# Optimization experiments

Measured on AMD Instinct MI355X. Metric: run time of the kernel, lower is better.

Reference implementation:

```python
import jax, jax.numpy as jnp
import numpy as np

TEMP = 0.2
EPS = 1e-12  # F.normalize eps


def setup_inputs() -> dict:
    key = jax.random.key(0)
    k1, k2 = jax.random.split(key)
    l, B, K, D = 4, 64, 32, 128
    emb_i = jax.random.normal(k1, (l, B, K, D), dtype=jnp.float32)
    emb_j = jax.random.normal(k2, (l, B, K, D), dtype=jnp.float32)
    joint_valid = jnp.ones((B, K), dtype=jnp.float32)
    return {"emb_i": emb_i, "emb_j": emb_j, "joint_valid": joint_valid}


def _l2norm(x):
    n = jnp.sqrt(jnp.sum(x * x, axis=-1, keepdims=True))
    return x / jnp.maximum(n, EPS)


def reference(emb_i, emb_j, joint_valid):
    l, B, K, D = emb_i.shape
    N = B * K
    z_i = _l2norm(emb_i.reshape(l, N, D))
    z_j = _l2norm(emb_j.reshape(l, N, D))
    reps = jnp.concatenate([z_i, z_j], axis=1)              # (l, 2N, D), unit rows
    # cosine similarity of unit vectors == matmul
    sim = jnp.einsum('lnd,lmd->lnm', reps, reps)            # (l, 2N, 2N)
    idx = jnp.arange(N)
    pos = sim[:, idx, idx + N]                              # diag offset +N, (l, N)
    # note: original code uses the SAME +N offset diagonal for both ij and ji
    positives = jnp.concatenate([pos, pos], axis=1)         # (l, 2N)
    neg_mask = 1.0 - jnp.eye(2 * N, dtype=sim.dtype)        # (2N, 2N)
    denom = jnp.sum(neg_mask[None] * jnp.exp(sim / TEMP), axis=2)  # (l, 2N)
    loss_partial = -jnp.log(jnp.exp(positives / TEMP) / denom)    # (l, 2N)
    joints_mask = joint_valid.reshape(1, 1, B, K)
    all_num = jnp.sum(joint_valid)
    loss = jnp.sum(loss_partial.reshape(l, 2, B, K) * joints_mask) / (2.0 * all_num)
    return loss
```

## Files before the change

kernel.cpp:

```cpp
#include <hip/hip_runtime.h>
#include <hip/hip_bf16.h>

typedef __attribute__((ext_vector_type(8))) short short8;
typedef __attribute__((ext_vector_type(4))) float floatx4;

#define NROWS 4096
#define NHALF 2048
#define DDIM  128
#define LDST  136
#define SQRT_SCALE 2.6857914f
#define LN2 0.69314718056f

#define WS_ROWSUM_OFF 64
#define WS_DIAG_OFF   16448
#define WS_POS_OFF    32832
#define WS_Z_BYTE_OFF 196864

__device__ inline unsigned short f2bf(float f) {
    unsigned u = __builtin_bit_cast(unsigned, f);
    u += 0x7fffu + ((u >> 16) & 1u);
    return (unsigned short)(u >> 16);
}

__global__ __launch_bounds__(256) void k_norm(const float* __restrict__ emb_i,
                                              const float* __restrict__ emb_j,
                                              const float* __restrict__ jv,
                                              float* __restrict__ wsf,
                                              unsigned short* __restrict__ z) {
    int bx = blockIdx.x, tid = threadIdx.x;
    if (bx == 4096) {
        __shared__ float sred[256];
        float s = 0.f;
        #pragma unroll
        for (int i = 0; i < 8; ++i) s += jv[tid + 256 * i];
        sred[tid] = s; __syncthreads();
        for (int off = 128; off > 0; off >>= 1) {
            if (tid < off) sred[tid] += sred[tid + off];
            __syncthreads();
        }
        if (tid == 0) wsf[1] = sred[0];
        return;
    }
    int gid = bx * 256 + tid;
    if (gid == 0) wsf[0] = 0.f;
    if (gid >= WS_ROWSUM_OFF && gid < WS_ROWSUM_OFF + 16384) wsf[gid] = 0.f;

    int wave = tid >> 6, lane = tid & 63;
    int r = bx * 4 + wave;
    int l = r >> 12, n = r & 4095;
    const float* src = (n < NHALF) ? (emb_i + ((size_t)l * NHALF + n) * DDIM)
                                   : (emb_j + ((size_t)l * NHALF + (n - NHALF)) * DDIM);
    float2 v = *(const float2*)(src + lane * 2);
    float ss = v.x * v.x + v.y * v.y;
    #pragma unroll
    for (int off = 1; off < 64; off <<= 1) ss += __shfl_xor(ss, off);
    float inv = SQRT_SCALE / fmaxf(sqrtf(ss), 1e-12f);
    unsigned pack = ((unsigned)f2bf(v.y * inv) << 16) | (unsigned)f2bf(v.x * inv);
    *(unsigned*)(z + (size_t)r * DDIM + lane * 2) = pack;
}

__global__ __launch_bounds__(256) void k_sim(const unsigned short* __restrict__ z,
                                             float* __restrict__ rowsum,
                                             float* __restrict__ diag,
                                             float* __restrict__ pos) {
    __shared__ __align__(16) unsigned short lds[128 * LDST];
    int bx = blockIdx.x, tid = threadIdx.x;
    int l = bx & 3, rb = (bx >> 2) & 15, cb = bx >> 6;
    int wave = tid >> 6, lane = tid & 63, m = lane & 15, quad = lane >> 4;
    const unsigned short* zl = z + (size_t)l * NROWS * DDIM;
    int l4 = l * NROWS;
    int wr0 = rb * 256 + wave * 64;

    short8 a[4][4];
    #pragma unroll
    for (int rs = 0; rs < 4; ++rs) {
        const unsigned short* p = zl + (size_t)(wr0 + rs * 16 + m) * DDIM + quad * 8;
        #pragma unroll
        for (int kk = 0; kk < 4; ++kk) a[rs][kk] = *(const short8*)(p + kk * 32);
    }
    floatx4 rsum[4];
    #pragma unroll
    for (int rs = 0; rs < 4; ++rs) rsum[rs] = (floatx4){0.f, 0.f, 0.f, 0.f};

    for (int stg = 0; stg < 4; ++stg) {
        int cg0 = cb * 512 + stg * 128;
        __syncthreads();
        #pragma unroll
        for (int i = 0; i < 8; ++i) {
            int chunk = tid + 256 * i;
            int col = chunk >> 4, off = chunk & 15;
            uint4 d = *(const uint4*)(zl + (size_t)(cg0 + col) * DDIM + off * 8);
            *(uint4*)&lds[col * LDST + off * 8] = d;
        }
        __syncthreads();
        #pragma unroll
        for (int cs = 0; cs < 8; ++cs) {
            int ct = cg0 + cs * 16;
            const unsigned short* lp = &lds[(cs * 16 + m) * LDST + quad * 8];
            short8 b0 = *(const short8*)(lp);
            short8 b1 = *(const short8*)(lp + 32);
            short8 b2 = *(const short8*)(lp + 64);
            short8 b3 = *(const short8*)(lp + 96);
            #pragma unroll
            for (int rs = 0; rs < 4; ++rs) {
                floatx4 acc = (floatx4){0.f, 0.f, 0.f, 0.f};
                acc = __builtin_amdgcn_mfma_f32_16x16x32_bf16(a[rs][0], b0, acc, 0, 0, 0);
                acc = __builtin_amdgcn_mfma_f32_16x16x32_bf16(a[rs][1], b1, acc, 0, 0, 0);
                acc = __builtin_amdgcn_mfma_f32_16x16x32_bf16(a[rs][2], b2, acc, 0, 0, 0);
                acc = __builtin_amdgcn_mfma_f32_16x16x32_bf16(a[rs][3], b3, acc, 0, 0, 0);
                int rowbase = wr0 + rs * 16;
                bool isdiag = (ct == rowbase);
                bool ispos  = (ct == (rowbase ^ 2048));
                if (isdiag || ispos) {
                    int c = m - (quad << 2);
                    if (c >= 0 && c < 4) {
                        float v = acc[c];
                        float* dst = isdiag ? &diag[l4 + rowbase + m]
                                            : &pos[l4 + rowbase + m];
                        *dst = v;
                    }
                }
                #pragma unroll
                for (int c = 0; c < 4; ++c)
                    rsum[rs][c] += __builtin_amdgcn_exp2f(acc[c]);
            }
        }
    }
    #pragma unroll
    for (int off = 1; off < 16; off <<= 1)
        #pragma unroll
        for (int rs = 0; rs < 4; ++rs)
            #pragma unroll
            for (int c = 0; c < 4; ++c)
                rsum[rs][c] += __shfl_xor(rsum[rs][c], off);
    if (m == 0) {
        #pragma unroll
        for (int rs = 0; rs < 4; ++rs)
            #pragma unroll
            for (int c = 0; c < 4; ++c) {
                int rg = wr0 + rs * 16 + quad * 4 + c;
                atomicAdd(&rowsum[l4 + rg], rsum[rs][c]);
            }
    }
}

__global__ __launch_bounds__(256) void k_loss(const float* __restrict__ jv,
                                              const float* __restrict__ rowsum,
                                              const float* __restrict__ diag,
                                              const float* __restrict__ pos,
                                              float* __restrict__ wsf) {
    __shared__ float sred[256];
    int tid = threadIdx.x;
    int r = blockIdx.x * 256 + tid;
    int n = r & 4095;
    float denom = rowsum[r] - __builtin_amdgcn_exp2f(diag[r]);
    float contrib = LN2 * (__builtin_amdgcn_logf(denom) - pos[r]);
    float local = contrib * jv[n & (NHALF - 1)];
    sred[tid] = local; __syncthreads();
    for (int off = 128; off > 0; off >>= 1) {
        if (tid < off) sred[tid] += sred[tid + off];
        __syncthreads();
    }
    if (tid == 0) atomicAdd(&wsf[0], sred[0]);
}

__global__ void k_final(const float* __restrict__ wsf, float* __restrict__ out) {
    if (threadIdx.x == 0) out[0] = wsf[0] / (2.f * wsf[1]);
}

extern "C" void kernel_launch(void* const* d_in, const int* in_sizes, int n_in,
                              void* d_out, int out_size, void* d_ws, size_t ws_size,
                              hipStream_t stream) {
    const float* emb_i = (const float*)d_in[0];
    const float* emb_j = (const float*)d_in[1];
    const float* jv    = (const float*)d_in[2];
    float* wsf    = (float*)d_ws;
    float* rowsum = wsf + WS_ROWSUM_OFF;
    float* diag   = wsf + WS_DIAG_OFF;
    float* pos    = wsf + WS_POS_OFF;
    unsigned short* z = (unsigned short*)((char*)d_ws + WS_Z_BYTE_OFF);
    float* out = (float*)d_out;

    k_norm <<<4097, 256, 0, stream>>>(emb_i, emb_j, jv, wsf, z);
    k_sim  <<<512,  256, 0, stream>>>(z, rowsum, diag, pos);
    k_loss <<<64,   256, 0, stream>>>(jv, rowsum, diag, pos, wsf);
    k_final<<<1,    64,  0, stream>>>(wsf, out);
}
```

Baseline: 99.83 us.

## Exploit similarity symmetry by computing only upper-triangular tiles with column sums

The similarity kernel now enumerates only the upper-triangular 256x256 tiles per layer. Each off-diagonal tile adds its exp values both into row sums and, through LDS atomics, into column sums, so each mirrored tile is computed once. This roughly halves the MFMA and exp work, at the cost of extra shuffles and shared and global atomics. The normalize kernel also processes two rows per wave with float4 loads to cut its block count.

```diff
diff --git a/kernel.cpp b/kernel.cpp
--- a/kernel.cpp
+++ b/kernel.cpp
@@ -28,7 +28,7 @@
                                               float* __restrict__ wsf,
                                               unsigned short* __restrict__ z) {
     int bx = blockIdx.x, tid = threadIdx.x;
-    if (bx == 4096) {
+    if (bx == 2048) {
         __shared__ float sred[256];
         float s = 0.f;
         #pragma unroll
@@ -45,18 +45,19 @@
     if (gid == 0) wsf[0] = 0.f;
     if (gid >= WS_ROWSUM_OFF && gid < WS_ROWSUM_OFF + 16384) wsf[gid] = 0.f;
 
-    int wave = tid >> 6, lane = tid & 63;
-    int r = bx * 4 + wave;
+    int wave = tid >> 6, lane = tid & 63, half = lane >> 5, sl = lane & 31;
+    int r = bx * 8 + wave * 2 + half;
     int l = r >> 12, n = r & 4095;
     const float* src = (n < NHALF) ? (emb_i + ((size_t)l * NHALF + n) * DDIM)
                                    : (emb_j + ((size_t)l * NHALF + (n - NHALF)) * DDIM);
-    float2 v = *(const float2*)(src + lane * 2);
-    float ss = v.x * v.x + v.y * v.y;
-    #pragma unroll
-    for (int off = 1; off < 64; off <<= 1) ss += __shfl_xor(ss, off);
+    float4 v = *(const float4*)(src + sl * 4);
+    float ss = v.x * v.x + v.y * v.y + v.z * v.z + v.w * v.w;
+    #pragma unroll
+    for (int off = 1; off < 32; off <<= 1) ss += __shfl_xor(ss, off);
     float inv = SQRT_SCALE / fmaxf(sqrtf(ss), 1e-12f);
-    unsigned pack = ((unsigned)f2bf(v.y * inv) << 16) | (unsigned)f2bf(v.x * inv);
-    *(unsigned*)(z + (size_t)r * DDIM + lane * 2) = pack;
+    unsigned p0 = ((unsigned)f2bf(v.y * inv) << 16) | (unsigned)f2bf(v.x * inv);
+    unsigned p1 = ((unsigned)f2bf(v.w * inv) << 16) | (unsigned)f2bf(v.z * inv);
+    *(uint2*)(z + (size_t)r * DDIM + sl * 4) = (uint2){p0, p1};
 }
 
 __global__ __launch_bounds__(256) void k_sim(const unsigned short* __restrict__ z,
@@ -64,12 +65,21 @@
                                              float* __restrict__ diag,
                                              float* __restrict__ pos) {
     __shared__ __align__(16) unsigned short lds[128 * LDST];
+    __shared__ float colsum[256];
     int bx = blockIdx.x, tid = threadIdx.x;
-    int l = bx & 3, rb = (bx >> 2) & 15, cb = bx >> 6;
+    int l = bx & 3, t = bx >> 2;
+    int rb = 0;
+    while (t >= 16 - rb) { t -= 16 - rb; ++rb; }
+    int cb = rb + t;
+    bool offdiag = (cb != rb);
+    bool isposT  = (cb == (rb ^ 8));
+    int R = rb * 256, C = cb * 256;
     int wave = tid >> 6, lane = tid & 63, m = lane & 15, quad = lane >> 4;
     const unsigned short* zl = z + (size_t)l * NROWS * DDIM;
     int l4 = l * NROWS;
-    int wr0 = rb * 256 + wave * 64;
+    int wr0 = R + wave * 64;
+
+    colsum[tid] = 0.f;
 
     short8 a[4][4];
     #pragma unroll
@@ -82,8 +92,8 @@
     #pragma unroll
     for (int rs = 0; rs < 4; ++rs) rsum[rs] = (floatx4){0.f, 0.f, 0.f, 0.f};
 
-    for (int stg = 0; stg < 4; ++stg) {
-        int cg0 = cb * 512 + stg * 128;
+    for (int stg = 0; stg < 2; ++stg) {
+        int cg0 = C + stg * 128;
         __syncthreads();
         #pragma unroll
         for (int i = 0; i < 8; ++i) {
@@ -95,12 +105,13 @@
         __syncthreads();
         #pragma unroll
         for (int cs = 0; cs < 8; ++cs) {
-            int ct = cg0 + cs * 16;
+            int lc = stg * 128 + cs * 16;
             const unsigned short* lp = &lds[(cs * 16 + m) * LDST + quad * 8];
             short8 b0 = *(const short8*)(lp);
             short8 b1 = *(const short8*)(lp + 32);
             short8 b2 = *(const short8*)(lp + 64);
             short8 b3 = *(const short8*)(lp + 96);
+            float cacc = 0.f;
             #pragma unroll
             for (int rs = 0; rs < 4; ++rs) {
                 floatx4 acc = (floatx4){0.f, 0.f, 0.f, 0.f};
@@ -108,21 +119,30 @@
                 acc = __builtin_amdgcn_mfma_f32_16x16x32_bf16(a[rs][1], b1, acc, 0, 0, 0);
                 acc = __builtin_amdgcn_mfma_f32_16x16x32_bf16(a[rs][2], b2, acc, 0, 0, 0);
                 acc = __builtin_amdgcn_mfma_f32_16x16x32_bf16(a[rs][3], b3, acc, 0, 0, 0);
-                int rowbase = wr0 + rs * 16;
-                bool isdiag = (ct == rowbase);
-                bool ispos  = (ct == (rowbase ^ 2048));
-                if (isdiag || ispos) {
+                int lr = wave * 64 + rs * 16;
+                if (lr == lc) {
                     int c = m - (quad << 2);
                     if (c >= 0 && c < 4) {
                         float v = acc[c];
-                        float* dst = isdiag ? &diag[l4 + rowbase + m]
-                                            : &pos[l4 + rowbase + m];
-                        *dst = v;
+                        if (!offdiag) diag[l4 + R + lr + m] = v;
+                        else if (isposT) {
+                            pos[l4 + R + lr + m] = v;
+                            pos[l4 + C + lr + m] = v;
+                        }
                     }
                 }
-                #pragma unroll
-                for (int c = 0; c < 4; ++c)
-                    rsum[rs][c] += __builtin_amdgcn_exp2f(acc[c]);
+                float e0 = __builtin_amdgcn_exp2f(acc[0]);
+                float e1 = __builtin_amdgcn_exp2f(acc[1]);
+                float e2 = __builtin_amdgcn_exp2f(acc[2]);
+                float e3 = __builtin_amdgcn_exp2f(acc[3]);
+                rsum[rs][0] += e0; rsum[rs][1] += e1;
+                rsum[rs][2] += e2; rsum[rs][3] += e3;
+                cacc += (e0 + e1) + (e2 + e3);
+            }
+            if (offdiag) {
+                cacc += __shfl_xor(cacc, 16);
+                cacc += __shfl_xor(cacc, 32);
+                if (quad == 0) atomicAdd(&colsum[lc + m], cacc);
             }
         }
     }
@@ -141,6 +161,10 @@
                 int rg = wr0 + rs * 16 + quad * 4 + c;
                 atomicAdd(&rowsum[l4 + rg], rsum[rs][c]);
             }
+    }
+    if (offdiag) {
+        __syncthreads();
+        atomicAdd(&rowsum[l4 + C + tid], colsum[tid]);
     }
 }
 
@@ -181,8 +205,8 @@
     unsigned short* z = (unsigned short*)((char*)d_ws + WS_Z_BYTE_OFF);
     float* out = (float*)d_out;
 
-    k_norm <<<4097, 256, 0, stream>>>(emb_i, emb_j, jv, wsf, z);
-    k_sim  <<<512,  256, 0, stream>>>(z, rowsum, diag, pos);
+    k_norm <<<2049, 256, 0, stream>>>(emb_i, emb_j, jv, wsf, z);
+    k_sim  <<<544,  256, 0, stream>>>(z, rowsum, diag, pos);
     k_loss <<<64,   256, 0, stream>>>(jv, rowsum, diag, pos, wsf);
     k_final<<<1,    64,  0, stream>>>(wsf, out);
 }
```

Measured after the change: 104.3 us. 1.04x slower.

## Drop LDS staging in sim kernel, prefetch B from global, replace atomics with partials

Applied to the files above, without the earlier changes.

The similarity kernel no longer stages column tiles through shared memory with barriers. Each wave now loads its B fragments directly from global memory (L2-resident) and double-buffers them with a register prefetch of the next 16-column slab. Row-sum atomics are replaced by per-column-group partial sums that the loss kernel adds up, which removes the zeroing pass in the norm kernel. The norm kernel also processes two rows per wave with float4 loads. The trade-off is that each wave reloads B redundantly from cache and uses more workspace.

```diff
diff --git a/kernel.cpp b/kernel.cpp
--- a/kernel.cpp
+++ b/kernel.cpp
@@ -7,14 +7,13 @@
 #define NROWS 4096
 #define NHALF 2048
 #define DDIM  128
-#define LDST  136
 #define SQRT_SCALE 2.6857914f
 #define LN2 0.69314718056f
 
-#define WS_ROWSUM_OFF 64
-#define WS_DIAG_OFF   16448
-#define WS_POS_OFF    32832
-#define WS_Z_BYTE_OFF 196864
+#define WS_ROWPART_OFF 64
+#define WS_DIAG_OFF   131136
+#define WS_POS_OFF    147520
+#define WS_Z_BYTE_OFF 655616
 
 __device__ inline unsigned short f2bf(float f) {
     unsigned u = __builtin_bit_cast(unsigned, f);
@@ -28,7 +27,7 @@
                                               float* __restrict__ wsf,
                                               unsigned short* __restrict__ z) {
     int bx = blockIdx.x, tid = threadIdx.x;
-    if (bx == 4096) {
+    if (bx == 2048) {
         __shared__ float sred[256];
         float s = 0.f;
         #pragma unroll
@@ -41,40 +40,39 @@
         if (tid == 0) wsf[1] = sred[0];
         return;
     }
-    int gid = bx * 256 + tid;
-    if (gid == 0) wsf[0] = 0.f;
-    if (gid >= WS_ROWSUM_OFF && gid < WS_ROWSUM_OFF + 16384) wsf[gid] = 0.f;
+    if (bx == 0 && tid == 0) wsf[0] = 0.f;
 
-    int wave = tid >> 6, lane = tid & 63;
-    int r = bx * 4 + wave;
+    int wave = tid >> 6, lane = tid & 63, half = lane >> 5, sl = lane & 31;
+    int r = bx * 8 + wave * 2 + half;
     int l = r >> 12, n = r & 4095;
     const float* src = (n < NHALF) ? (emb_i + ((size_t)l * NHALF + n) * DDIM)
                                    : (emb_j + ((size_t)l * NHALF + (n - NHALF)) * DDIM);
-    float2 v = *(const float2*)(src + lane * 2);
-    float ss = v.x * v.x + v.y * v.y;
+    float4 v = *(const float4*)(src + sl * 4);
+    float ss = v.x * v.x + v.y * v.y + v.z * v.z + v.w * v.w;
     #pragma unroll
-    for (int off = 1; off < 64; off <<= 1) ss += __shfl_xor(ss, off);
+    for (int off = 1; off < 32; off <<= 1) ss += __shfl_xor(ss, off);
     float inv = SQRT_SCALE / fmaxf(sqrtf(ss), 1e-12f);
-    unsigned pack = ((unsigned)f2bf(v.y * inv) << 16) | (unsigned)f2bf(v.x * inv);
-    *(unsigned*)(z + (size_t)r * DDIM + lane * 2) = pack;
+    unsigned p0 = ((unsigned)f2bf(v.y * inv) << 16) | (unsigned)f2bf(v.x * inv);
+    unsigned p1 = ((unsigned)f2bf(v.w * inv) << 16) | (unsigned)f2bf(v.z * inv);
+    *(uint2*)(z + (size_t)r * DDIM + sl * 4) = (uint2){p0, p1};
 }
 
 __global__ __launch_bounds__(256) void k_sim(const unsigned short* __restrict__ z,
-                                             float* __restrict__ rowsum,
+                                             float* __restrict__ rowpart,
                                              float* __restrict__ diag,
                                              float* __restrict__ pos) {
-    __shared__ __align__(16) unsigned short lds[128 * LDST];
     int bx = blockIdx.x, tid = threadIdx.x;
-    int l = bx & 3, rb = (bx >> 2) & 15, cb = bx >> 6;
+    int l = bx & 3, rb = (bx >> 2) & 15, cg = bx >> 6;
     int wave = tid >> 6, lane = tid & 63, m = lane & 15, quad = lane >> 4;
     const unsigned short* zl = z + (size_t)l * NROWS * DDIM;
     int l4 = l * NROWS;
-    int wr0 = rb * 256 + wave * 64;
+    int R0 = rb * 256 + wave * 64;
+    int C0 = cg * 512;
 
     short8 a[4][4];
     #pragma unroll
     for (int rs = 0; rs < 4; ++rs) {
-        const unsigned short* p = zl + (size_t)(wr0 + rs * 16 + m) * DDIM + quad * 8;
+        const unsigned short* p = zl + (size_t)(R0 + rs * 16 + m) * DDIM + quad * 8;
         #pragma unroll
         for (int kk = 0; kk < 4; ++kk) a[rs][kk] = *(const short8*)(p + kk * 32);
     }
@@ -82,48 +80,40 @@
     #pragma unroll
     for (int rs = 0; rs < 4; ++rs) rsum[rs] = (floatx4){0.f, 0.f, 0.f, 0.f};
 
-    for (int stg = 0; stg < 4; ++stg) {
-        int cg0 = cb * 512 + stg * 128;
-        __syncthreads();
+    const unsigned short* bp = zl + (size_t)(C0 + m) * DDIM + quad * 8;
+    short8 bc[4], bn[4];
+    #pragma unroll
+    for (int k = 0; k < 4; ++k) bc[k] = *(const short8*)(bp + k * 32);
+
+    #pragma unroll 2
+    for (int cs = 0; cs < 32; ++cs) {
+        if (cs < 31) {
+            const unsigned short* q = bp + (size_t)(cs + 1) * 16 * DDIM;
+            #pragma unroll
+            for (int k = 0; k < 4; ++k) bn[k] = *(const short8*)(q + k * 32);
+        }
+        int c0 = C0 + cs * 16;
         #pragma unroll
-        for (int i = 0; i < 8; ++i) {
-            int chunk = tid + 256 * i;
-            int col = chunk >> 4, off = chunk & 15;
-            uint4 d = *(const uint4*)(zl + (size_t)(cg0 + col) * DDIM + off * 8);
-            *(uint4*)&lds[col * LDST + off * 8] = d;
+        for (int rs = 0; rs < 4; ++rs) {
+            floatx4 acc = (floatx4){0.f, 0.f, 0.f, 0.f};
+            acc = __builtin_amdgcn_mfma_f32_16x16x32_bf16(a[rs][0], bc[0], acc, 0, 0, 0);
+            acc = __builtin_amdgcn_mfma_f32_16x16x32_bf16(a[rs][1], bc[1], acc, 0, 0, 0);
+            acc = __builtin_amdgcn_mfma_f32_16x16x32_bf16(a[rs][2], bc[2], acc, 0, 0, 0);
+            acc = __builtin_amdgcn_mfma_f32_16x16x32_bf16(a[rs][3], bc[3], acc, 0, 0, 0);
+            int rbase = R0 + rs * 16;
+            if (c0 == rbase || c0 == (rbase ^ 2048)) {
+                int c = m - (quad << 2);
+                if (c >= 0 && c < 4)
+                    ((c0 == rbase) ? diag : pos)[l4 + rbase + m] = acc[c];
+            }
+            rsum[rs][0] += __builtin_amdgcn_exp2f(acc[0]);
+            rsum[rs][1] += __builtin_amdgcn_exp2f(acc[1]);
+            rsum[rs][2] += __builtin_amdgcn_exp2f(acc[2]);
+            rsum[rs][3] += __builtin_amdgcn_exp2f(acc[3]);
         }
-        __syncthreads();
-        #pragma unroll
-        for (int cs = 0; cs < 8; ++cs) {
-            int ct = cg0 + cs * 16;
-            const unsigned short* lp = &lds[(cs * 16 + m) * LDST + quad * 8];
-            short8 b0 = *(const short8*)(lp);
-            short8 b1 = *(const short8*)(lp + 32);
-            short8 b2 = *(const short8*)(lp + 64);
-            short8 b3 = *(const short8*)(lp + 96);
+        if (cs < 31) {
             #pragma unroll
-            for (int rs = 0; rs < 4; ++rs) {
-                floatx4 acc = (floatx4){0.f, 0.f, 0.f, 0.f};
-                acc = __builtin_amdgcn_mfma_f32_16x16x32_bf16(a[rs][0], b0, acc, 0, 0, 0);
-                acc = __builtin_amdgcn_mfma_f32_16x16x32_bf16(a[rs][1], b1, acc, 0, 0, 0);
-                acc = __builtin_amdgcn_mfma_f32_16x16x32_bf16(a[rs][2], b2, acc, 0, 0, 0);
-                acc = __builtin_amdgcn_mfma_f32_16x16x32_bf16(a[rs][3], b3, acc, 0, 0, 0);
-                int rowbase = wr0 + rs * 16;
-                bool isdiag = (ct == rowbase);
-                bool ispos  = (ct == (rowbase ^ 2048));
-                if (isdiag || ispos) {
-                    int c = m - (quad << 2);
-                    if (c >= 0 && c < 4) {
-                        float v = acc[c];
-                        float* dst = isdiag ? &diag[l4 + rowbase + m]
-                                            : &pos[l4 + rowbase + m];
-                        *dst = v;
-                    }
-                }
-                #pragma unroll
-                for (int c = 0; c < 4; ++c)
-                    rsum[rs][c] += __builtin_amdgcn_exp2f(acc[c]);
-            }
+            for (int k = 0; k < 4; ++k) bc[k] = bn[k];
         }
     }
     #pragma unroll
@@ -138,14 +128,14 @@
         for (int rs = 0; rs < 4; ++rs)
             #pragma unroll
             for (int c = 0; c < 4; ++c) {
-                int rg = wr0 + rs * 16 + quad * 4 + c;
-                atomicAdd(&rowsum[l4 + rg], rsum[rs][c]);
+                int rg = R0 + rs * 16 + quad * 4 + c;
+                rowpart[cg * 16384 + l4 + rg] = rsum[rs][c];
             }
     }
 }
 
 __global__ __launch_bounds__(256) void k_loss(const float* __restrict__ jv,
-                                              const float* __restrict__ rowsum,
+                                              const float* __restrict__ rowpart,
                                               const float* __restrict__ diag,
                                               const float* __restrict__ pos,
                                               float* __restrict__ wsf) {
@@ -153,7 +143,10 @@
     int tid = threadIdx.x;
     int r = blockIdx.x * 256 + tid;
     int n = r & 4095;
-    float denom = rowsum[r] - __builtin_amdgcn_exp2f(diag[r]);
+    float tot = 0.f;
+    #pragma unroll
+    for (int g = 0; g < 8; ++g) tot += rowpart[g * 16384 + r];
+    float denom = tot - __builtin_amdgcn_exp2f(diag[r]);
     float contrib = LN2 * (__builtin_amdgcn_logf(denom) - pos[r]);
     float local = contrib * jv[n & (NHALF - 1)];
     sred[tid] = local; __syncthreads();
@@ -174,15 +167,15 @@
     const float* emb_i = (const float*)d_in[0];
     const float* emb_j = (const float*)d_in[1];
     const float* jv    = (const float*)d_in[2];
-    float* wsf    = (float*)d_ws;
-    float* rowsum = wsf + WS_ROWSUM_OFF;
-    float* diag   = wsf + WS_DIAG_OFF;
-    float* pos    = wsf + WS_POS_OFF;
+    float* wsf     = (float*)d_ws;
+    float* rowpart = wsf + WS_ROWPART_OFF;
+    float* diag    = wsf + WS_DIAG_OFF;
+    float* pos     = wsf + WS_POS_OFF;
     unsigned short* z = (unsigned short*)((char*)d_ws + WS_Z_BYTE_OFF);
     float* out = (float*)d_out;
 
-    k_norm <<<4097, 256, 0, stream>>>(emb_i, emb_j, jv, wsf, z);
-    k_sim  <<<512,  256, 0, stream>>>(z, rowsum, diag, pos);
-    k_loss <<<64,   256, 0, stream>>>(jv, rowsum, diag, pos, wsf);
+    k_norm <<<2049, 256, 0, stream>>>(emb_i, emb_j, jv, wsf, z);
+    k_sim  <<<512,  256, 0, stream>>>(z, rowpart, diag, pos);
+    k_loss <<<64,   256, 0, stream>>>(jv, rowpart, diag, pos, wsf);
     k_final<<<1,    64,  0, stream>>>(wsf, out);
 }
```

New measurement: 102.6 us. +2.8%, slower.
